# Optimization experiments

Measured on AMD Instinct MI355X. Metric: run time of the kernel, lower is better.

Reference implementation:

```python
import jax, jax.numpy as jnp
import numpy as np

KH, KW, STRIDE, PAD, DIL = 3, 3, 1, 1, 1


def setup_inputs() -> dict:
    key = jax.random.key(0)
    k1, k2, k3, k4, k5 = jax.random.split(key, 5)
    B, Cin, H, W = 8, 64, 128, 128
    Cout = 64
    K = KH * KW
    Ho = (H + 2 * PAD - DIL * (KH - 1) - 1) // STRIDE + 1
    Wo = (W + 2 * PAD - DIL * (KW - 1) - 1) // STRIDE + 1
    return {
        "input": jax.random.normal(k1, (B, Cin, H, W), dtype=jnp.float32),
        "offset": jax.random.normal(k2, (B, 2 * K, Ho, Wo), dtype=jnp.float32),
        "mask": jax.random.uniform(k3, (B, K, Ho, Wo), dtype=jnp.float32),
        "weight": jax.random.normal(k4, (Cout, Cin, KH, KW), dtype=jnp.float32) * 0.05,
        "bias": jax.random.normal(k5, (Cout,), dtype=jnp.float32) * 0.01,
    }


def _bilinear_gather(xb, py, px):
    # xb: [C,H,W]; py/px: [K,Ho,Wo] fractional sample coords. Zero padding outside.
    C, H, W = xb.shape
    y0 = jnp.floor(py)
    x0 = jnp.floor(px)
    wy = py - y0
    wx = px - x0

    def g(yi, xi):
        yi = yi.astype(jnp.int32)
        xi = xi.astype(jnp.int32)
        valid = ((yi >= 0) & (yi < H) & (xi >= 0) & (xi < W)).astype(xb.dtype)
        yc = jnp.clip(yi, 0, H - 1)
        xc = jnp.clip(xi, 0, W - 1)
        return xb[:, yc, xc] * valid[None]  # [C,K,Ho,Wo]

    return (g(y0, x0) * ((1 - wy) * (1 - wx))[None]
            + g(y0, x0 + 1) * ((1 - wy) * wx)[None]
            + g(y0 + 1, x0) * (wy * (1 - wx))[None]
            + g(y0 + 1, x0 + 1) * (wy * wx)[None])


def _deform_conv2d(x, offset, mask, weight, bias):
    B, Cin, H, W = x.shape
    Cout = weight.shape[0]
    K = KH * KW
    _, _, Ho, Wo = mask.shape
    # base sampling grid per kernel tap
    kh = jnp.arange(KH)
    kw = jnp.arange(KW)
    base_y = (jnp.arange(Ho) * STRIDE - PAD)[None, :] + (kh * DIL)[:, None]  # [KH,Ho]
    base_x = (jnp.arange(Wo) * STRIDE - PAD)[None, :] + (kw * DIL)[:, None]  # [KW,Wo]
    base_y = jnp.repeat(base_y, KW, axis=0)              # [K,Ho]
    base_x = jnp.tile(base_x, (KH, 1))                   # [K,Wo]
    off = offset.reshape(B, K, 2, Ho, Wo)                # torchvision layout: (y,x) per tap
    py = base_y[None, :, :, None].astype(x.dtype) + off[:, :, 0]  # [B,K,Ho,Wo]
    px = base_x[None, :, None, :].astype(x.dtype) + off[:, :, 1]
    sampled = jax.vmap(_bilinear_gather)(x, py, px)      # [B,Cin,K,Ho,Wo]
    sampled = sampled * mask[:, None]                    # modulated (DCNv2)
    w = weight.reshape(Cout, Cin, K)
    out = jnp.einsum('bckhw,ock->bohw', sampled, w) + bias[None, :, None, None]
    return out


def reference(input, offset, mask, weight, bias):
    out = _deform_conv2d(input, offset, mask, weight, bias)
    return jnp.clip(out, 0.0, 6.0)  # ReLU6
```

## Files before the change

### kernel.cpp

```cpp
#include <hip/hip_runtime.h>

typedef __attribute__((ext_vector_type(8))) short short8;
typedef __attribute__((ext_vector_type(8))) unsigned short ushort8;
typedef __attribute__((ext_vector_type(4))) float floatx4;

constexpr int B = 8, Cin = 64, Hh = 128, Ww = 128, Cout = 64, Kt = 9, Ho = 128, Wo = 128;

__device__ __forceinline__ unsigned short f2bf(float f) {
    unsigned int u = __float_as_uint(f);
    unsigned int r = (u + 0x7fffu + ((u >> 16) & 1u)) >> 16;
    return (unsigned short)r;
}
__device__ __forceinline__ float bf2f(unsigned short s) {
    return __uint_as_float((unsigned int)s << 16);
}

__global__ void prep_w(const float* __restrict__ w, unsigned short* __restrict__ wA) {
    int i = blockIdx.x * 256 + threadIdx.x;
    if (i >= Cout * Cin * Kt) return;
    int o = i / (Cin * Kt);
    int r = i % (Cin * Kt);
    int c = r / Kt;
    int k = r % Kt;
    wA[o * 576 + k * 64 + c] = f2bf(w[i]);
}

__global__ __launch_bounds__(256) void to_nhwc(const float* __restrict__ in,
                                               unsigned short* __restrict__ xn) {
    __shared__ float s[64 * 65];
    const int t = threadIdx.x;
    const int blk = blockIdx.x;
    const int b = blk >> 8;
    const int y = (blk & 255) >> 1;
    const int x0 = (blk & 1) * 64;
    const float* src = in + ((size_t)(b * 64) * 128 + y) * 128 + x0;
    #pragma unroll
    for (int i = 0; i < 16; ++i) {
        int c = i * 4 + (t >> 6);
        s[c * 65 + (t & 63)] = src[(size_t)c * 16384 + (t & 63)];
    }
    __syncthreads();
    const int x = t >> 2, c0 = (t & 3) * 16;
    ushort8 o0, o1;
    #pragma unroll
    for (int j = 0; j < 8; ++j) {
        o0[j] = f2bf(s[(c0 + j) * 65 + x]);
        o1[j] = f2bf(s[(c0 + 8 + j) * 65 + x]);
    }
    unsigned short* dst = xn + (((size_t)(b * 128 + y) * 128 + x0 + x) * 64 + c0);
    *(ushort8*)dst = o0;
    *(ushort8*)(dst + 8) = o1;
}

__global__ __launch_bounds__(256) void dcn_mfma(
    const unsigned short* __restrict__ xn, const float* __restrict__ off,
    const float* __restrict__ msk, const unsigned short* __restrict__ wA,
    const float* __restrict__ bias, float* __restrict__ out) {
    __shared__ unsigned short s_b[64 * 64];

    const int t = threadIdx.x;
    int blk = blockIdx.x;
    blk = (blk & 7) * 256 + (blk >> 3);
    const int b = blk >> 8;
    const int ho = (blk & 255) >> 1;
    const int w0 = (blk & 1) * 64;

    const int wv = t >> 6;
    const int l = t & 63;

    const int p = t >> 2;
    const int cg = t & 3;
    const int wo = w0 + p;

    floatx4 acc[4] = {};

    const unsigned short* wbase = wA + (16 * wv + (l & 15)) * 576 + (l >> 4) * 8;
    const unsigned short* xb = xn + (size_t)b * (128 * 128 * 64) + cg * 16;

    for (int k = 0; k < Kt; ++k) {
        short8 a0 = *(const short8*)(wbase + k * 64);
        short8 a1 = *(const short8*)(wbase + k * 64 + 32);

        {
            const int kh = k / 3, kw = k - kh * 3;
            const size_t obase = ((size_t)b * 18 + 2 * k) * 16384 + ho * 128 + wo;
            const float oy = off[obase];
            const float ox = off[obase + 16384];
            const float m = msk[((size_t)b * 9 + k) * 16384 + ho * 128 + wo];
            const float py = (float)(ho - 1 + kh) + oy;
            const float px = (float)(wo - 1 + kw) + ox;
            const float y0f = floorf(py), x0f = floorf(px);
            const int iy0 = (int)y0f, ix0 = (int)x0f;
            const float wy = py - y0f, wx = px - x0f;
            const int iy1 = iy0 + 1, ix1 = ix0 + 1;
            const bool vy0 = ((unsigned)iy0 < 128u), vy1 = ((unsigned)iy1 < 128u);
            const bool vx0 = ((unsigned)ix0 < 128u), vx1 = ((unsigned)ix1 < 128u);
            float w00 = (1.f - wy) * (1.f - wx) * m * ((vy0 && vx0) ? 1.f : 0.f);
            float w01 = (1.f - wy) * wx * m * ((vy0 && vx1) ? 1.f : 0.f);
            float w10 = wy * (1.f - wx) * m * ((vy1 && vx0) ? 1.f : 0.f);
            float w11 = wy * wx * m * ((vy1 && vx1) ? 1.f : 0.f);
            const int cy0 = min(max(iy0, 0), 127), cy1 = min(max(iy1, 0), 127);
            const int cx0 = min(max(ix0, 0), 127), cx1 = min(max(ix1, 0), 127);
            const unsigned short* p00 = xb + ((size_t)cy0 * 128 + cx0) * 64;
            const unsigned short* p01 = xb + ((size_t)cy0 * 128 + cx1) * 64;
            const unsigned short* p10 = xb + ((size_t)cy1 * 128 + cx0) * 64;
            const unsigned short* p11 = xb + ((size_t)cy1 * 128 + cx1) * 64;
            ushort8 q00a = *(const ushort8*)p00, q00b = *(const ushort8*)(p00 + 8);
            ushort8 q01a = *(const ushort8*)p01, q01b = *(const ushort8*)(p01 + 8);
            ushort8 q10a = *(const ushort8*)p10, q10b = *(const ushort8*)(p10 + 8);
            ushort8 q11a = *(const ushort8*)p11, q11b = *(const ushort8*)(p11 + 8);
            ushort8 vA, vB;
            #pragma unroll
            for (int j = 0; j < 8; ++j) {
                float v = bf2f(q00a[j]) * w00 + bf2f(q01a[j]) * w01 +
                          bf2f(q10a[j]) * w10 + bf2f(q11a[j]) * w11;
                vA[j] = f2bf(v);
            }
            #pragma unroll
            for (int j = 0; j < 8; ++j) {
                float v = bf2f(q00b[j]) * w00 + bf2f(q01b[j]) * w01 +
                          bf2f(q10b[j]) * w10 + bf2f(q11b[j]) * w11;
                vB[j] = f2bf(v);
            }
            const int ckA = (cg * 2) ^ (p & 7);
            const int ckB = (cg * 2 + 1) ^ (p & 7);
            *(ushort8*)&s_b[p * 64 + ckA * 8] = vA;
            *(ushort8*)&s_b[p * 64 + ckB * 8] = vB;
        }
        __syncthreads();
        #pragma unroll
        for (int h = 0; h < 2; ++h) {
            short8 a = h ? a1 : a0;
            #pragma unroll
            for (int f = 0; f < 4; ++f) {
                const int pp = 16 * f + (l & 15);
                const int ck = (h * 4 + (l >> 4)) ^ (pp & 7);
                short8 bfrag = *(const short8*)&s_b[pp * 64 + ck * 8];
                acc[f] = __builtin_amdgcn_mfma_f32_16x16x32_bf16(a, bfrag, acc[f], 0, 0, 0);
            }
        }
        __syncthreads();
    }

    #pragma unroll
    for (int f = 0; f < 4; ++f) {
        #pragma unroll
        for (int r = 0; r < 4; ++r) {
            const int co = 16 * wv + (l >> 4) * 4 + r;
            float v = acc[f][r] + bias[co];
            v = fminf(fmaxf(v, 0.f), 6.f);
            out[(((size_t)b * 64 + co) * 128 + ho) * 128 + w0 + 16 * f + (l & 15)] = v;
        }
    }
}

constexpr int NT = 64;
constexpr int LDSS = 68;

__global__ void reorder_weight(const float* __restrict__ w, float* __restrict__ wT) {
    int i = blockIdx.x * blockDim.x + threadIdx.x;
    if (i >= Cout * Cin * Kt) return;
    int o = i / (Cin * Kt);
    int r = i % (Cin * Kt);
    int c = r / Kt;
    int k = r % Kt;
    wT[(k * Cin + c) * Cout + o] = w[i];
}

__global__ __launch_bounds__(256, 4) void dcn_kernel(
    const float* __restrict__ in, const float* __restrict__ off,
    const float* __restrict__ msk, const float* __restrict__ wT,
    const float* __restrict__ bias, float* __restrict__ out) {
    __shared__ float s_w[Cin * LDSS];
    __shared__ float s_s[Cin * LDSS];
    const int tid = threadIdx.x;
    const int blk = blockIdx.x;
    const int b = blk >> 8;
    const int ho = (blk & 255) >> 1;
    const int w0 = (blk & 1) * NT;
    const int lane = tid & 63;
    const int c4 = tid >> 6;
    const int ty = tid >> 4;
    const int tx = tid & 15;
    const float* in_b = in + b * (Cin * Hh * Ww);
    const int wo = w0 + lane;
    float acc[4][4];
    #pragma unroll
    for (int i = 0; i < 4; ++i)
        #pragma unroll
        for (int j = 0; j < 4; ++j) acc[i][j] = 0.f;
    for (int k = 0; k < Kt; ++k) {
        {
            const float* src = wT + k * (Cin * Cout);
            const int c = tid >> 2;
            const int g = tid & 3;
            const float4* s = (const float4*)(src + c * Cout + g * 16);
            float4* dq = (float4*)(&s_w[c * LDSS + g * 16]);
            dq[0] = s[0]; dq[1] = s[1]; dq[2] = s[2]; dq[3] = s[3];
        }
        {
            const int kh = k / 3, kw = k % 3;
            const float oy = off[(((size_t)b * 2 * Kt + 2 * k) * Ho + ho) * Wo + wo];
            const float ox = off[(((size_t)b * 2 * Kt + 2 * k + 1) * Ho + ho) * Wo + wo];
            const float m = msk[(((size_t)b * Kt + k) * Ho + ho) * Wo + wo];
            const float py = (float)(ho - 1 + kh) + oy;
            const float px = (float)(wo - 1 + kw) + ox;
            const float y0f = floorf(py), x0f = floorf(px);
            const int iy0 = (int)y0f, ix0 = (int)x0f;
            const float wy = py - y0f, wx = px - x0f;
            const int iy1 = iy0 + 1, ix1 = ix0 + 1;
            const bool vy0 = (iy0 >= 0) & (iy0 < Hh);
            const bool vy1 = (iy1 >= 0) & (iy1 < Hh);
            const bool vx0 = (ix0 >= 0) & (ix0 < Ww);
            const bool vx1 = (ix1 >= 0) & (ix1 < Ww);
            const int cy0 = min(max(iy0, 0), Hh - 1), cy1 = min(max(iy1, 0), Hh - 1);
            const int cx0 = min(max(ix0, 0), Ww - 1), cx1 = min(max(ix1, 0), Ww - 1);
            const float w00 = (1.f - wy) * (1.f - wx) * m * ((vy0 & vx0) ? 1.f : 0.f);
            const float w01 = (1.f - wy) * wx * m * ((vy0 & vx1) ? 1.f : 0.f);
            const float w10 = wy * (1.f - wx) * m * ((vy1 & vx0) ? 1.f : 0.f);
            const float w11 = wy * wx * m * ((vy1 & vx1) ? 1.f : 0.f);
            const int o00 = cy0 * Ww + cx0, o01 = cy0 * Ww + cx1;
            const int o10 = cy1 * Ww + cx0, o11 = cy1 * Ww + cx1;
            const float* pp = in_b + (c4 * 16) * (Hh * Ww);
            #pragma unroll
            for (int ii = 0; ii < 16; ++ii) {
                float v = pp[o00] * w00 + pp[o01] * w01 + pp[o10] * w10 + pp[o11] * w11;
                s_s[(c4 * 16 + ii) * LDSS + lane] = v;
                pp += Hh * Ww;
            }
        }
        __syncthreads();
        #pragma unroll 8
        for (int c = 0; c < Cin; ++c) {
            const float4 a = *(const float4*)(&s_w[c * LDSS + ty * 4]);
            const float4 bv = *(const float4*)(&s_s[c * LDSS + tx * 4]);
            const float* ap = (const float*)&a;
            const float* bp = (const float*)&bv;
            #pragma unroll
            for (int i = 0; i < 4; ++i)
                #pragma unroll
                for (int j = 0; j < 4; ++j) acc[i][j] += ap[i] * bp[j];
        }
        __syncthreads();
    }
    #pragma unroll
    for (int i = 0; i < 4; ++i) {
        const int co = ty * 4 + i;
        const float bs = bias[co];
        float4 r;
        float* rp = (float*)&r;
        #pragma unroll
        for (int j = 0; j < 4; ++j) {
            float v = acc[i][j] + bs;
            v = fminf(fmaxf(v, 0.f), 6.f);
            rp[j] = v;
        }
        *(float4*)(&out[(((size_t)b * Cout + co) * Ho + ho) * Wo + w0 + tx * 4]) = r;
    }
}

extern "C" void kernel_launch(void* const* d_in, const int* in_sizes, int n_in,
                              void* d_out, int out_size, void* d_ws, size_t ws_size,
                              hipStream_t stream) {
    const float* in = (const float*)d_in[0];
    const float* off = (const float*)d_in[1];
    const float* msk = (const float*)d_in[2];
    const float* w = (const float*)d_in[3];
    const float* bias = (const float*)d_in[4];
    float* out = (float*)d_out;

    const size_t needX = (size_t)8 * 128 * 128 * 64 * 2;
    const size_t xoff = 131072;
    if (ws_size >= xoff + needX) {
        unsigned short* wAb = (unsigned short*)d_ws;
        unsigned short* xnb = (unsigned short*)((char*)d_ws + xoff);
        prep_w<<<144, 256, 0, stream>>>(w, wAb);
        to_nhwc<<<2048, 256, 0, stream>>>(in, xnb);
        dcn_mfma<<<2048, 256, 0, stream>>>(xnb, off, msk, wAb, bias, out);
    } else {
        float* wT = (float*)d_ws;
        reorder_weight<<<(Cout * Cin * Kt + 255) / 256, 256, 0, stream>>>(w, wT);
        dcn_kernel<<<(B * Ho * Wo) / NT, 256, 0, stream>>>(in, off, msk, wT, bias, out);
    }
}
```

Measured before the change: 63.84 us.

## Precompute bilinear metadata in LDS and use packed bf16 dot2 interpolation

Sampling metadata (bf16-packed bilinear weights with the mask folded in, and 16-bit corner offsets) is computed once per block for all 9 taps and stored in shared memory. Previously each of the four threads sharing a pixel recomputed it. The interpolation now uses byte permutes plus v_dot2_f32_bf16 and v_cvt_pk_bf16_f32 in place of scalar bf16-to-float conversions, FMAs and software rounding. LDS read offsets are hoisted out of the tap loop. Rounding the interpolation weights to bf16 adds a small precision loss, and the prologue adds a barrier and some LDS use.

```diff
diff --git a/kernel.cpp b/kernel.cpp
--- a/kernel.cpp
+++ b/kernel.cpp
@@ -3,6 +3,7 @@
 typedef __attribute__((ext_vector_type(8))) short short8;
 typedef __attribute__((ext_vector_type(8))) unsigned short ushort8;
 typedef __attribute__((ext_vector_type(4))) float floatx4;
+typedef __attribute__((ext_vector_type(4))) unsigned int uintx4;
 
 constexpr int B = 8, Cin = 64, Hh = 128, Ww = 128, Cout = 64, Kt = 9, Ho = 128, Wo = 128;
 
@@ -11,8 +12,16 @@
     unsigned int r = (u + 0x7fffu + ((u >> 16) & 1u)) >> 16;
     return (unsigned short)r;
 }
-__device__ __forceinline__ float bf2f(unsigned short s) {
-    return __uint_as_float((unsigned int)s << 16);
+
+__device__ __forceinline__ unsigned int cvtpk(float lo, float hi) {
+    unsigned int r;
+    asm("v_cvt_pk_bf16_f32 %0, %1, %2" : "=v"(r) : "v"(lo), "v"(hi));
+    return r;
+}
+__device__ __forceinline__ float dot2bf(unsigned int a, unsigned int b, float c) {
+    float d;
+    asm("v_dot2_f32_bf16 %0, %1, %2, %3" : "=v"(d) : "v"(a), "v"(b), "v"(c));
+    return d;
 }
 
 __global__ void prep_w(const float* __restrict__ w, unsigned short* __restrict__ wA) {
@@ -56,6 +65,7 @@
     const unsigned short* __restrict__ xn, const float* __restrict__ off,
     const float* __restrict__ msk, const unsigned short* __restrict__ wA,
     const float* __restrict__ bias, float* __restrict__ out) {
+    __shared__ uintx4 s_meta[Kt * 64];
     __shared__ unsigned short s_b[64 * 64];
 
     const int t = threadIdx.x;
@@ -67,75 +77,106 @@
 
     const int wv = t >> 6;
     const int l = t & 63;
-
     const int p = t >> 2;
     const int cg = t & 3;
-    const int wo = w0 + p;
+
+    for (int idx = t; idx < Kt * 64; idx += 256) {
+        const int k = idx >> 6, pp = idx & 63;
+        const int kh = k / 3, kw = k - kh * 3;
+        const int wo = w0 + pp;
+        const size_t obase = ((size_t)b * 18 + 2 * k) * 16384 + ho * 128 + wo;
+        const float oy = off[obase];
+        const float ox = off[obase + 16384];
+        const float m = msk[((size_t)b * 9 + k) * 16384 + ho * 128 + wo];
+        const float py = (float)(ho - 1 + kh) + oy;
+        const float px = (float)(wo - 1 + kw) + ox;
+        const float y0f = floorf(py), x0f = floorf(px);
+        const int iy0 = (int)y0f, ix0 = (int)x0f;
+        const float wy = py - y0f, wx = px - x0f;
+        const int iy1 = iy0 + 1, ix1 = ix0 + 1;
+        const bool vy0 = ((unsigned)iy0 < 128u), vy1 = ((unsigned)iy1 < 128u);
+        const bool vx0 = ((unsigned)ix0 < 128u), vx1 = ((unsigned)ix1 < 128u);
+        const float w00 = (1.f - wy) * (1.f - wx) * m * ((vy0 && vx0) ? 1.f : 0.f);
+        const float w01 = (1.f - wy) * wx * m * ((vy0 && vx1) ? 1.f : 0.f);
+        const float w10 = wy * (1.f - wx) * m * ((vy1 && vx0) ? 1.f : 0.f);
+        const float w11 = wy * wx * m * ((vy1 && vx1) ? 1.f : 0.f);
+        const int cy0 = min(max(iy0, 0), 127), cy1 = min(max(iy1, 0), 127);
+        const int cx0 = min(max(ix0, 0), 127), cx1 = min(max(ix1, 0), 127);
+        const unsigned o00 = (unsigned)(cy0 * 128 + cx0), o01 = (unsigned)(cy0 * 128 + cx1);
+        const unsigned o10 = (unsigned)(cy1 * 128 + cx0), o11 = (unsigned)(cy1 * 128 + cx1);
+        uintx4 mt;
+        mt.x = cvtpk(w00, w01);
+        mt.y = cvtpk(w10, w11);
+        mt.z = o00 | (o01 << 16);
+        mt.w = o10 | (o11 << 16);
+        s_meta[idx] = mt;
+    }
+    __syncthreads();
 
     floatx4 acc[4] = {};
 
     const unsigned short* wbase = wA + (16 * wv + (l & 15)) * 576 + (l >> 4) * 8;
     const unsigned short* xb = xn + (size_t)b * (128 * 128 * 64) + cg * 16;
+    const int ckA = (cg * 2) ^ (p & 7);
+    const int ckB = (cg * 2 + 1) ^ (p & 7);
+    unsigned short* wrA = &s_b[p * 64 + ckA * 8];
+    unsigned short* wrB = &s_b[p * 64 + ckB * 8];
+    int rdo[8];
+    #pragma unroll
+    for (int h = 0; h < 2; ++h)
+        #pragma unroll
+        for (int f = 0; f < 4; ++f) {
+            const int pp = 16 * f + (l & 15);
+            const int ck = (h * 4 + (l >> 4)) ^ (pp & 7);
+            rdo[h * 4 + f] = pp * 64 + ck * 8;
+        }
 
     for (int k = 0; k < Kt; ++k) {
-        short8 a0 = *(const short8*)(wbase + k * 64);
-        short8 a1 = *(const short8*)(wbase + k * 64 + 32);
-
-        {
-            const int kh = k / 3, kw = k - kh * 3;
-            const size_t obase = ((size_t)b * 18 + 2 * k) * 16384 + ho * 128 + wo;
-            const float oy = off[obase];
-            const float ox = off[obase + 16384];
-            const float m = msk[((size_t)b * 9 + k) * 16384 + ho * 128 + wo];
-            const float py = (float)(ho - 1 + kh) + oy;
-            const float px = (float)(wo - 1 + kw) + ox;
-            const float y0f = floorf(py), x0f = floorf(px);
-            const int iy0 = (int)y0f, ix0 = (int)x0f;
-            const float wy = py - y0f, wx = px - x0f;
-            const int iy1 = iy0 + 1, ix1 = ix0 + 1;
-            const bool vy0 = ((unsigned)iy0 < 128u), vy1 = ((unsigned)iy1 < 128u);
-            const bool vx0 = ((unsigned)ix0 < 128u), vx1 = ((unsigned)ix1 < 128u);
-            float w00 = (1.f - wy) * (1.f - wx) * m * ((vy0 && vx0) ? 1.f : 0.f);
-            float w01 = (1.f - wy) * wx * m * ((vy0 && vx1) ? 1.f : 0.f);
-            float w10 = wy * (1.f - wx) * m * ((vy1 && vx0) ? 1.f : 0.f);
-            float w11 = wy * wx * m * ((vy1 && vx1) ? 1.f : 0.f);
-            const int cy0 = min(max(iy0, 0), 127), cy1 = min(max(iy1, 0), 127);
-            const int cx0 = min(max(ix0, 0), 127), cx1 = min(max(ix1, 0), 127);
-            const unsigned short* p00 = xb + ((size_t)cy0 * 128 + cx0) * 64;
-            const unsigned short* p01 = xb + ((size_t)cy0 * 128 + cx1) * 64;
-            const unsigned short* p10 = xb + ((size_t)cy1 * 128 + cx0) * 64;
-            const unsigned short* p11 = xb + ((size_t)cy1 * 128 + cx1) * 64;
-            ushort8 q00a = *(const ushort8*)p00, q00b = *(const ushort8*)(p00 + 8);
-            ushort8 q01a = *(const ushort8*)p01, q01b = *(const ushort8*)(p01 + 8);
-            ushort8 q10a = *(const ushort8*)p10, q10b = *(const ushort8*)(p10 + 8);
-            ushort8 q11a = *(const ushort8*)p11, q11b = *(const ushort8*)(p11 + 8);
-            ushort8 vA, vB;
-            #pragma unroll
-            for (int j = 0; j < 8; ++j) {
-                float v = bf2f(q00a[j]) * w00 + bf2f(q01a[j]) * w01 +
-                          bf2f(q10a[j]) * w10 + bf2f(q11a[j]) * w11;
-                vA[j] = f2bf(v);
-            }
-            #pragma unroll
-            for (int j = 0; j < 8; ++j) {
-                float v = bf2f(q00b[j]) * w00 + bf2f(q01b[j]) * w01 +
-                          bf2f(q10b[j]) * w10 + bf2f(q11b[j]) * w11;
-                vB[j] = f2bf(v);
-            }
-            const int ckA = (cg * 2) ^ (p & 7);
-            const int ckB = (cg * 2 + 1) ^ (p & 7);
-            *(ushort8*)&s_b[p * 64 + ckA * 8] = vA;
-            *(ushort8*)&s_b[p * 64 + ckB * 8] = vB;
-        }
+        const short8 a0 = *(const short8*)(wbase + k * 64);
+        const short8 a1 = *(const short8*)(wbase + k * 64 + 32);
+
+        const uintx4 mt = s_meta[k * 64 + p];
+        const unsigned wp01 = mt.x, wp23 = mt.y;
+        const uintx4* c00 = (const uintx4*)(xb + ((size_t)(mt.z & 0xffffu) << 6));
+        const uintx4* c01 = (const uintx4*)(xb + ((size_t)(mt.z >> 16) << 6));
+        const uintx4* c10 = (const uintx4*)(xb + ((size_t)(mt.w & 0xffffu) << 6));
+        const uintx4* c11 = (const uintx4*)(xb + ((size_t)(mt.w >> 16) << 6));
+        const uintx4 q00a = c00[0], q00b = c00[1];
+        const uintx4 q01a = c01[0], q01b = c01[1];
+        const uintx4 q10a = c10[0], q10b = c10[1];
+        const uintx4 q11a = c11[0], q11b = c11[1];
+
+        uintx4 vA, vB;
+        #pragma unroll
+        for (int j = 0; j < 4; ++j) {
+            const unsigned pa = __builtin_amdgcn_perm(q01a[j], q00a[j], 0x05040100u);
+            const unsigned pb = __builtin_amdgcn_perm(q11a[j], q10a[j], 0x05040100u);
+            const unsigned pc = __builtin_amdgcn_perm(q01a[j], q00a[j], 0x07060302u);
+            const unsigned pd = __builtin_amdgcn_perm(q11a[j], q10a[j], 0x07060302u);
+            const float f0 = dot2bf(pa, wp01, dot2bf(pb, wp23, 0.f));
+            const float f1 = dot2bf(pc, wp01, dot2bf(pd, wp23, 0.f));
+            vA[j] = cvtpk(f0, f1);
+        }
+        #pragma unroll
+        for (int j = 0; j < 4; ++j) {
+            const unsigned pa = __builtin_amdgcn_perm(q01b[j], q00b[j], 0x05040100u);
+            const unsigned pb = __builtin_amdgcn_perm(q11b[j], q10b[j], 0x05040100u);
+            const unsigned pc = __builtin_amdgcn_perm(q01b[j], q00b[j], 0x07060302u);
+            const unsigned pd = __builtin_amdgcn_perm(q11b[j], q10b[j], 0x07060302u);
+            const float f0 = dot2bf(pa, wp01, dot2bf(pb, wp23, 0.f));
+            const float f1 = dot2bf(pc, wp01, dot2bf(pd, wp23, 0.f));
+            vB[j] = cvtpk(f0, f1);
+        }
+        *(uintx4*)wrA = vA;
+        *(uintx4*)wrB = vB;
         __syncthreads();
+
         #pragma unroll
         for (int h = 0; h < 2; ++h) {
-            short8 a = h ? a1 : a0;
+            const short8 a = h ? a1 : a0;
             #pragma unroll
             for (int f = 0; f < 4; ++f) {
-                const int pp = 16 * f + (l & 15);
-                const int ck = (h * 4 + (l >> 4)) ^ (pp & 7);
-                short8 bfrag = *(const short8*)&s_b[pp * 64 + ck * 8];
+                const short8 bfrag = *(const short8*)&s_b[rdo[h * 4 + f]];
                 acc[f] = __builtin_amdgcn_mfma_f32_16x16x32_bf16(a, bfrag, acc[f], 0, 0, 0);
             }
         }
```

Measured after the change: 61.14 us. -4.2%, faster.
